# Kernel optimization log

Hardware: AMD Instinct MI355X
Metric: run time of the kernel (lower is better)

## Reference

```python
import jax, jax.numpy as jnp
import numpy as np

B, S, IN, OUT = 4, 2048, 4096, 4096


def setup_inputs() -> dict:
    key = jax.random.key(0)
    k_x, k_q, k_s, k_z, k_b = jax.random.split(key, 5)
    x = jax.random.normal(k_x, (B, S, IN), dtype=jnp.float32)
    # packed int4 weights: each int holds two unsigned nibbles (inputs 2r and 2r+1)
    qweight = jax.random.randint(k_q, (IN // 2, OUT), 0, 256, dtype=jnp.int32)
    # per-output-channel scales (positive) and zeros (zeros = zero_point * scale in pack())
    scales = jax.random.uniform(k_s, (OUT, 1), minval=0.01, maxval=0.05, dtype=jnp.float32)
    zeros = jax.random.normal(k_z, (OUT, 1), dtype=jnp.float32) * 0.1
    bias = jax.random.normal(k_b, (OUT,), dtype=jnp.float32) * 0.02
    return {"x": x, "qweight": qweight, "scales": scales, "zeros": zeros, "bias": bias}


def _dequant_weight(qweight, scales, zeros):
    # unpack two 4-bit values per packed element along the input dim
    low = qweight & 0xF            # input index 2r
    high = (qweight >> 4) & 0xF    # input index 2r+1
    w_int = jnp.stack([low, high], axis=1).reshape(-1, qweight.shape[1])  # (IN, OUT)
    zp = jnp.round(zeros / scales)  # integer zero point per output channel, (OUT,1)
    # w = (q - zp) * scale, broadcast per output column
    return (w_int.astype(jnp.float32) - zp.T) * scales.T  # (IN, OUT)


def reference(x, qweight, scales, zeros, bias):
    w = _dequant_weight(qweight, scales, zeros)          # (IN, OUT) fp32
    y = jnp.einsum('bsi,io->bso', x.astype(jnp.float32), w) + bias
    return y.astype(x.dtype)
```

## Files before the change

kernel.cpp:

```cpp
#include <hip/hip_runtime.h>
#include <hip/hip_bf16.h>
#include <stdint.h>

#define M_TOT 8192
#define N_TOT 4096
#define K_TOT 4096
#define BM 128
#define BN 128
#define BKI 128
#define NTI (K_TOT / BKI)

typedef short s16x8 __attribute__((ext_vector_type(8)));
typedef float f32x4 __attribute__((ext_vector_type(4)));
typedef int   i32x4 __attribute__((ext_vector_type(4)));
typedef char  i8x16 __attribute__((ext_vector_type(16)));
typedef unsigned int u32;

__device__ __forceinline__ short f2bf(float f) {
    unsigned int u = __float_as_uint(f);
    u = (u + 0x7fffu + ((u >> 16) & 1u)) >> 16;
    return (short)u;
}

__device__ __forceinline__ void async_copy16(const void* g, void* l) {
    __builtin_amdgcn_global_load_lds(
        (const __attribute__((address_space(1))) void*)g,
        (__attribute__((address_space(3))) void*)l, 16, 0, 0);
}

__global__ __launch_bounds__(256)
void prep(const float* __restrict__ x, const int* __restrict__ qw,
          char* __restrict__ xq, char* __restrict__ wq,
          float* __restrict__ sxv, float* __restrict__ sumv) {
    __shared__ float rmax[4], rsum[4];
    __shared__ char tile[256 * 64];
    const int t = threadIdx.x;

    if (blockIdx.x < M_TOT) {
        const int row = blockIdx.x;
        const float* xp = x + (size_t)row * K_TOT + t * 16;
        f32x4 f[4];
        float amax = 0.f, sum = 0.f;
        #pragma unroll
        for (int i = 0; i < 4; ++i) {
            f[i] = *(const f32x4*)(xp + i * 4);
            #pragma unroll
            for (int j = 0; j < 4; ++j) {
                amax = fmaxf(amax, fabsf(f[i][j]));
                sum += f[i][j];
            }
        }
        #pragma unroll
        for (int s = 1; s < 64; s <<= 1) {
            amax = fmaxf(amax, __shfl_xor(amax, s, 64));
            sum += __shfl_xor(sum, s, 64);
        }
        const int wv = t >> 6;
        if ((t & 63) == 0) { rmax[wv] = amax; rsum[wv] = sum; }
        __syncthreads();
        amax = fmaxf(fmaxf(rmax[0], rmax[1]), fmaxf(rmax[2], rmax[3]));
        sum  = rsum[0] + rsum[1] + rsum[2] + rsum[3];
        const float inv = amax > 0.f ? 127.0f / amax : 0.f;
        i8x16 v;
        #pragma unroll
        for (int i = 0; i < 4; ++i)
            #pragma unroll
            for (int j = 0; j < 4; ++j)
                v[i * 4 + j] = (char)(int)rintf(f[i][j] * inv);
        *(i8x16*)&xq[(size_t)row * K_TOT + t * 16] = v;
        if (t == 0) { sxv[row] = amax * (1.0f / 127.0f); sumv[row] = sum; }
    } else {
        const int bq = blockIdx.x - M_TOT;
        const int o0 = (bq & 15) * 256;
        const int kb = bq >> 4;
        const int r0 = kb * 32;
        const int o  = o0 + t;
        #pragma unroll
        for (int g = 0; g < 4; ++g) {
            i8x16 v;
            #pragma unroll
            for (int p = 0; p < 8; ++p) {
                const int q = qw[(size_t)(r0 + g * 8 + p) * N_TOT + o];
                v[2 * p]     = (char)(q & 15);
                v[2 * p + 1] = (char)((q >> 4) & 15);
            }
            *(i8x16*)&tile[t * 64 + ((g ^ (t & 3)) << 4)] = v;
        }
        __syncthreads();
        #pragma unroll
        for (int it = 0; it < 4; ++it) {
            const int L = it * 256 + t;
            const int row = L >> 2, c = L & 3;
            *(i8x16*)&wq[(size_t)(o0 + row) * K_TOT + kb * 64 + c * 16] =
                *(const i8x16*)&tile[row * 64 + ((c ^ (row & 3)) << 4)];
        }
    }
}

__global__ __launch_bounds__(256, 2)
void gemm_i8(const char* __restrict__ xq, const char* __restrict__ wq,
             const float* __restrict__ sxv, const float* __restrict__ sumv,
             const float* __restrict__ scales, const float* __restrict__ zeros,
             const float* __restrict__ bias, float* __restrict__ out) {
    __shared__ __align__(16) char Sm8[32768];
    char* As = Sm8;
    char* Bs = Sm8 + 16384;

    const int tid = threadIdx.x;
    const int n0 = blockIdx.x * BN;
    const int m0 = blockIdx.y * BM;
    const int lane = tid & 63;
    const int wv = tid >> 6;
    const int wr = wv >> 1, wc = wv & 1;
    const int lrow = lane & 15, lk = lane >> 4;

    i32x4 acc[4][4] = {};

    for (int kt = 0; kt < NTI; ++kt) {
        const int k0 = kt * BKI;
        #pragma unroll
        for (int i = 0; i < 4; ++i) {
            const int g = i * 256 + wv * 64 + lane;
            const int row = g >> 3, c = g & 7;
            async_copy16(xq + (size_t)(m0 + row) * K_TOT + k0 + ((c ^ (row & 7)) << 4),
                         &As[(i * 256 + wv * 64) * 16]);
        }
        #pragma unroll
        for (int i = 0; i < 4; ++i) {
            const int g = i * 256 + wv * 64 + lane;
            const int row = g >> 3, c = g & 7;
            async_copy16(wq + (size_t)(n0 + row) * K_TOT + k0 + ((c ^ (row & 7)) << 4),
                         &Bs[(i * 256 + wv * 64) * 16]);
        }
        __syncthreads();

        #pragma unroll
        for (int ks = 0; ks < 2; ++ks) {
            const int slot = ks * 4 + lk;
            i32x4 a[4], b[4];
            #pragma unroll
            for (int mi = 0; mi < 4; ++mi) {
                const int row = wr * 64 + mi * 16 + lrow;
                a[mi] = *(const i32x4*)&As[row * 128 + ((slot ^ (row & 7)) << 4)];
            }
            #pragma unroll
            for (int ni = 0; ni < 4; ++ni) {
                const int row = wc * 64 + ni * 16 + lrow;
                b[ni] = *(const i32x4*)&Bs[row * 128 + ((slot ^ (row & 7)) << 4)];
            }
            #pragma unroll
            for (int mi = 0; mi < 4; ++mi)
                #pragma unroll
                for (int ni = 0; ni < 4; ++ni)
                    acc[mi][ni] = __builtin_amdgcn_mfma_i32_16x16x64_i8(
                        a[mi], b[ni], acc[mi][ni], 0, 0, 0);
        }
        __syncthreads();
    }

    float* fbuf = (float*)Sm8;
    float c0v[4], c1v[4], bsv[4];
    #pragma unroll
    for (int ni = 0; ni < 4; ++ni) {
        const int cg = n0 + wc * 64 + ni * 16 + lrow;
        const float c0 = scales[cg];
        c0v[ni] = c0;
        c1v[ni] = -rintf(zeros[cg] / c0) * c0;
        bsv[ni] = bias[cg];
    }
    #pragma unroll
    for (int p = 0; p < 2; ++p) {
        __syncthreads();
        #pragma unroll
        for (int q = 0; q < 2; ++q) {
            const int mi = 2 * p + q;
            const int rl = wr * 32 + q * 16 + lk * 4;
            #pragma unroll
            for (int j = 0; j < 4; ++j) {
                const int r = rl + j;
                const int gr = m0 + wr * 64 + mi * 16 + lk * 4 + j;
                const float sx = sxv[gr];
                const float Sx = sumv[gr];
                #pragma unroll
                for (int ni = 0; ni < 4; ++ni) {
                    const int col = wc * 64 + ni * 16 + lrow;
                    const float y = fmaf(c0v[ni] * sx, (float)acc[mi][ni][j],
                                         fmaf(c1v[ni], Sx, bsv[ni]));
                    fbuf[r * 128 + (col ^ (((r >> 2) & 1) << 4))] = y;
                }
            }
        }
        __syncthreads();
        #pragma unroll
        for (int rd = 0; rd < 8; ++rd) {
            const int L = rd * 256 + tid;
            const int r = L >> 5;
            const int c4 = (L & 31) * 4;
            const float4 v = *(const float4*)&fbuf[r * 128 + (c4 ^ (((r >> 2) & 1) << 4))];
            const int grow = m0 + (r >> 5) * 64 + p * 32 + (r & 31);
            *(float4*)&out[(size_t)grow * N_TOT + n0 + c4] = v;
        }
    }
}

__global__ __launch_bounds__(256, 2)
void qlin_fused(const float* __restrict__ x,
                const int* __restrict__ qw,
                const float* __restrict__ scales,
                const float* __restrict__ zeros,
                const float* __restrict__ bias,
                float* __restrict__ out) {
    __shared__ short As[128 * 64];
    __shared__ short Bs[128 * 64];

    const int tid = threadIdx.x;
    const int n0 = blockIdx.x * 128;
    const int m0 = blockIdx.y * 128;

    const int a_kg   = tid & 7;
    const int a_row0 = tid >> 3;
    const int b_oloc = tid & 127;
    const int b_rg0  = tid >> 7;

    const int ocol = n0 + b_oloc;
    const float c0 = scales[ocol];
    const float c1 = -rintf(zeros[ocol] / c0) * c0;

    const int lane = tid & 63;
    const int wv   = tid >> 6;
    const int wr   = wv >> 1;
    const int wc   = wv & 1;
    const int lrow = lane & 15;
    const int lk   = lane >> 4;

    f32x4 acc[4][4] = {};

    for (int kt = 0; kt < K_TOT / 64; ++kt) {
        const int k0 = kt * 64;
        {
            const float* srcb = x + (size_t)(m0)*K_TOT + k0 + a_kg * 8;
            #pragma unroll
            for (int i = 0; i < 4; ++i) {
                const int row = a_row0 + 32 * i;
                const float4 f0 = *(const float4*)(srcb + (size_t)row * K_TOT);
                const float4 f1 = *(const float4*)(srcb + (size_t)row * K_TOT + 4);
                s16x8 v;
                v[0] = f2bf(f0.x); v[1] = f2bf(f0.y); v[2] = f2bf(f0.z); v[3] = f2bf(f0.w);
                v[4] = f2bf(f1.x); v[5] = f2bf(f1.y); v[6] = f2bf(f1.z); v[7] = f2bf(f1.w);
                *(s16x8*)&As[row * 64 + ((a_kg ^ (row & 7)) << 3)] = v;
            }
        }
        {
            const int rbase = k0 >> 1;
            #pragma unroll
            for (int i = 0; i < 4; ++i) {
                const int rg = b_rg0 + 2 * i;
                const int* qp = qw + (size_t)(rbase + rg * 4) * N_TOT + ocol;
                s16x8 v;
                #pragma unroll
                for (int rr = 0; rr < 4; ++rr) {
                    const int q = qp[(size_t)rr * N_TOT];
                    v[2 * rr]     = f2bf(fmaf((float)(q & 15), c0, c1));
                    v[2 * rr + 1] = f2bf(fmaf((float)((q >> 4) & 15), c0, c1));
                }
                *(s16x8*)&Bs[b_oloc * 64 + ((rg ^ (b_oloc & 7)) << 3)] = v;
            }
        }
        __syncthreads();
        #pragma unroll
        for (int ks = 0; ks < 2; ++ks) {
            const int slot = ks * 4 + lk;
            s16x8 a[4], b[4];
            #pragma unroll
            for (int mi = 0; mi < 4; ++mi) {
                const int row = wr * 64 + mi * 16 + lrow;
                a[mi] = *(const s16x8*)&As[row * 64 + ((slot ^ (row & 7)) << 3)];
            }
            #pragma unroll
            for (int ni = 0; ni < 4; ++ni) {
                const int row = wc * 64 + ni * 16 + lrow;
                b[ni] = *(const s16x8*)&Bs[row * 64 + ((slot ^ (row & 7)) << 3)];
            }
            #pragma unroll
            for (int mi = 0; mi < 4; ++mi)
                #pragma unroll
                for (int ni = 0; ni < 4; ++ni)
                    acc[mi][ni] = __builtin_amdgcn_mfma_f32_16x16x32_bf16(
                        a[mi], b[ni], acc[mi][ni], 0, 0, 0);
        }
        __syncthreads();
    }

    #pragma unroll
    for (int mi = 0; mi < 4; ++mi) {
        const int rg = m0 + wr * 64 + mi * 16 + lk * 4;
        #pragma unroll
        for (int ni = 0; ni < 4; ++ni) {
            const int cg = n0 + wc * 64 + ni * 16 + lrow;
            const float bs = bias[cg];
            #pragma unroll
            for (int j = 0; j < 4; ++j)
                out[(size_t)(rg + j) * N_TOT + cg] = acc[mi][ni][j] + bs;
        }
    }
}

extern "C" void kernel_launch(void* const* d_in, const int* in_sizes, int n_in,
                              void* d_out, int out_size, void* d_ws, size_t ws_size,
                              hipStream_t stream) {
    const float* x      = (const float*)d_in[0];
    const int*   qw     = (const int*)d_in[1];
    const float* scales = (const float*)d_in[2];
    const float* zeros  = (const float*)d_in[3];
    const float* bias   = (const float*)d_in[4];
    float* out = (float*)d_out;

    const size_t XQ_BYTES = (size_t)M_TOT * K_TOT;
    const size_t WQ_BYTES = (size_t)N_TOT * K_TOT;
    const size_t SX_BYTES = (size_t)M_TOT * 4;
    const size_t NEED = XQ_BYTES + WQ_BYTES + 2 * SX_BYTES;

    if (ws_size >= NEED) {
        char*  xq   = (char*)d_ws;
        char*  wqt  = (char*)d_ws + XQ_BYTES;
        float* sxv  = (float*)((char*)d_ws + XQ_BYTES + WQ_BYTES);
        float* sumv = sxv + M_TOT;

        hipLaunchKernelGGL(prep, dim3(M_TOT + 1024), dim3(256), 0, stream,
                           x, qw, xq, wqt, sxv, sumv);
        hipLaunchKernelGGL(gemm_i8, dim3(N_TOT / BN, M_TOT / BM), dim3(256), 0, stream,
                           xq, wqt, sxv, sumv, scales, zeros, bias, out);
    } else {
        hipLaunchKernelGGL(qlin_fused, dim3(N_TOT / 128, M_TOT / 128), dim3(256), 0, stream,
                           x, qw, scales, zeros, bias, out);
    }
}
```

Before: 174.2 us.

## Triple-buffer int8 GEMM main loop with async prefetch three tiles ahead

Replaces the single-buffered K loop (load tile, sync, compute, sync) with a three-stage LDS ring of 64-wide K tiles. Prefetches run three iterations ahead using vmcnt-based waits and raw barriers. The LDS swizzle changes to a rotation scheme for 64-byte rows, and MFMA issue is wrapped in s_setprio. This aims to hide global-load latency behind MFMA work, at the cost of more LDS (48KB), which may limit occupancy. It also adds redundant wraparound prefetches at the end of the loop.

```diff
diff --git a/kernel.cpp b/kernel.cpp
--- a/kernel.cpp
+++ b/kernel.cpp
@@ -7,7 +7,7 @@
 #define K_TOT 4096
 #define BM 128
 #define BN 128
-#define BKI 128
+#define BKI 64
 #define NTI (K_TOT / BKI)
 
 typedef short s16x8 __attribute__((ext_vector_type(8)));
@@ -102,10 +102,7 @@
              const float* __restrict__ sxv, const float* __restrict__ sumv,
              const float* __restrict__ scales, const float* __restrict__ zeros,
              const float* __restrict__ bias, float* __restrict__ out) {
-    __shared__ __align__(16) char Sm8[32768];
-    char* As = Sm8;
-    char* Bs = Sm8 + 16384;
-
+    __shared__ __align__(16) char Sm8[49152];
     const int tid = threadIdx.x;
     const int n0 = blockIdx.x * BN;
     const int m0 = blockIdx.y * BM;
@@ -116,47 +113,71 @@
 
     i32x4 acc[4][4] = {};
 
-    for (int kt = 0; kt < NTI; ++kt) {
-        const int k0 = kt * BKI;
-        #pragma unroll
-        for (int i = 0; i < 4; ++i) {
-            const int g = i * 256 + wv * 64 + lane;
-            const int row = g >> 3, c = g & 7;
-            async_copy16(xq + (size_t)(m0 + row) * K_TOT + k0 + ((c ^ (row & 7)) << 4),
-                         &As[(i * 256 + wv * 64) * 16]);
-        }
-        #pragma unroll
-        for (int i = 0; i < 4; ++i) {
-            const int g = i * 256 + wv * 64 + lane;
-            const int row = g >> 3, c = g & 7;
-            async_copy16(wq + (size_t)(n0 + row) * K_TOT + k0 + ((c ^ (row & 7)) << 4),
-                         &Bs[(i * 256 + wv * 64) * 16]);
-        }
-        __syncthreads();
-
-        #pragma unroll
-        for (int ks = 0; ks < 2; ++ks) {
-            const int slot = ks * 4 + lk;
-            i32x4 a[4], b[4];
-            #pragma unroll
-            for (int mi = 0; mi < 4; ++mi) {
-                const int row = wr * 64 + mi * 16 + lrow;
-                a[mi] = *(const i32x4*)&As[row * 128 + ((slot ^ (row & 7)) << 4)];
-            }
-            #pragma unroll
-            for (int ni = 0; ni < 4; ++ni) {
-                const int row = wc * 64 + ni * 16 + lrow;
-                b[ni] = *(const i32x4*)&Bs[row * 128 + ((slot ^ (row & 7)) << 4)];
-            }
-            #pragma unroll
-            for (int mi = 0; mi < 4; ++mi)
-                #pragma unroll
-                for (int ni = 0; ni < 4; ++ni)
-                    acc[mi][ni] = __builtin_amdgcn_mfma_i32_16x16x64_i8(
-                        a[mi], b[ni], acc[mi][ni], 0, 0, 0);
-        }
-        __syncthreads();
-    }
+    auto STAGE = [&](char* bufA, int tt) {
+        const int k0 = (tt & (NTI - 1)) * BKI;
+        char* bufB = bufA + 8192;
+        #pragma unroll
+        for (int i = 0; i < 2; ++i) {
+            const int L = i * 256 + tid;
+            const int row = L >> 2, c = L & 3;
+            const int sk = ((c - (row >> 1)) & 3) << 4;
+            async_copy16(xq + (size_t)(m0 + row) * K_TOT + k0 + sk,
+                         bufA + (i * 256 + wv * 64) * 16);
+        }
+        #pragma unroll
+        for (int i = 0; i < 2; ++i) {
+            const int L = i * 256 + tid;
+            const int row = L >> 2, c = L & 3;
+            const int sk = ((c - (row >> 1)) & 3) << 4;
+            async_copy16(wq + (size_t)(n0 + row) * K_TOT + k0 + sk,
+                         bufB + (i * 256 + wv * 64) * 16);
+        }
+    };
+
+    auto ITER = [&](char* bufCur, char* bufStage, int tt) {
+        asm volatile("s_waitcnt vmcnt(8)" ::: "memory");
+        __builtin_amdgcn_s_barrier();
+        char* bufB = bufCur + 8192;
+        i32x4 a[4], b[4];
+        #pragma unroll
+        for (int mi = 0; mi < 4; ++mi) {
+            const int row = wr * 64 + mi * 16 + lrow;
+            const int sp = (lk + (row >> 1)) & 3;
+            a[mi] = *(const i32x4*)&bufCur[row * 64 + sp * 16];
+        }
+        #pragma unroll
+        for (int ni = 0; ni < 4; ++ni) {
+            const int row = wc * 64 + ni * 16 + lrow;
+            const int sp = (lk + (row >> 1)) & 3;
+            b[ni] = *(const i32x4*)&bufB[row * 64 + sp * 16];
+        }
+        asm volatile("s_waitcnt lgkmcnt(0)" ::: "memory");
+        __builtin_amdgcn_s_barrier();
+        STAGE(bufStage, tt + 3);
+        __builtin_amdgcn_s_setprio(1);
+        #pragma unroll
+        for (int mi = 0; mi < 4; ++mi)
+            #pragma unroll
+            for (int ni = 0; ni < 4; ++ni)
+                acc[mi][ni] = __builtin_amdgcn_mfma_i32_16x16x64_i8(
+                    a[mi], b[ni], acc[mi][ni], 0, 0, 0);
+        __builtin_amdgcn_s_setprio(0);
+    };
+
+    char* const B0 = Sm8;
+    char* const B1 = Sm8 + 16384;
+    char* const B2 = Sm8 + 32768;
+
+    STAGE(B0, 0); STAGE(B1, 1); STAGE(B2, 2);
+
+    #pragma unroll 1
+    for (int t = 0; t < NTI - 1; t += 3) {
+        ITER(B0, B0, t);
+        ITER(B1, B1, t + 1);
+        ITER(B2, B2, t + 2);
+    }
+    ITER(B0, B0, NTI - 1);
+    asm volatile("s_waitcnt vmcnt(0)" ::: "memory");
 
     float* fbuf = (float*)Sm8;
     float c0v[4], c1v[4], bsv[4];
```

Result: slower. 208.4 us (+19.6%).
